# Optimization experiments

Hardware: AMD Instinct MI355X
Metric: run time of the kernel (lower is better)

The kernel has to match this reference:

```python
import jax, jax.numpy as jnp
import numpy as np

SIZE = 7
SIGMA = 1.5
K1 = 0.01
K2 = 0.03
DATA_RANGE = 2.0
NP_ = SIZE * SIZE
COV_NORM = NP_ / (NP_ - 1)
PAD = SIZE // 2


def _gaussian_window(size=SIZE, sigma=SIGMA, channels=1):
    x = np.arange(size) - size // 2
    g = np.exp(-x**2 / (2.0 * sigma**2))[None, :]
    g = (g.T @ g)
    g = g / g.sum()
    w = np.tile(g[None, None], (channels, 1, 1, 1))  # [C,1,size,size]
    return jnp.asarray(w, dtype=jnp.float32)


def _dwconv(x, w):
    # depthwise conv2d, zero padding PAD, stride 1; x: [N,C,H,W], w: [C,1,k,k]
    c = x.shape[1]
    return jax.lax.conv_general_dilated(
        x, w, window_strides=(1, 1), padding=[(PAD, PAD), (PAD, PAD)],
        dimension_numbers=('NCHW', 'OIHW', 'NCHW'), feature_group_count=c)


def setup_inputs() -> dict:
    key = jax.random.key(0)
    k1, k2 = jax.random.split(key)
    X = jax.random.uniform(k1, (64, 1, 320, 320), dtype=jnp.float32)
    Y = jax.random.uniform(k2, (64, 1, 320, 320), dtype=jnp.float32)
    window = _gaussian_window()
    return {"X": X, "Y": Y, "window": window}


def reference(X, Y, window):
    C1 = (K1 * DATA_RANGE) ** 2
    C2 = (K2 * DATA_RANGE) ** 2
    mux = _dwconv(X, window)
    muy = _dwconv(Y, window)
    mux_sq = mux * mux
    muy_sq = muy * muy
    muxy = mux * muy
    sigmax_sq = (_dwconv(X * X, window) - mux_sq) * COV_NORM
    sigmay_sq = (_dwconv(Y * Y, window) - muy_sq) * COV_NORM
    sigmaxy = (_dwconv(X * Y, window) - muxy) * COV_NORM
    ssim_map = ((2 * muxy + C1) * (2 * sigmaxy + C2)) / \
               ((mux_sq + muy_sq + C1) * (sigmax_sq + sigmay_sq + C2))
    return 1.0 - ssim_map.mean()
```

## Files before the change

kernel.cpp:

```cpp
#include <hip/hip_runtime.h>
#include <math.h>


#define WI 320
#define HI 320
#define NI 64
#define TWO 58
#define GXD 6
#define GYD 20
#define NBLK (GXD * GYD * NI)
#define NPIX ((double)NI * WI * HI)
#define WREG (5 * 4 * 64)

typedef float v4 __attribute__((ext_vector_type(4)));

struct W7 { float w[7]; };

template <bool YI, int XM>
__device__ __forceinline__ float wave_task(
    const float* __restrict__ Xn, const float* __restrict__ Yn,
    const W7& wv, float* __restrict__ vb, int x0, int y0, int lane)
{
    const int gx   = x0 + lane - 3;
    const bool xok = (XM == 1) || (XM == 0 ? (gx >= 0) : (gx < WI));

    float xr[10], yr[10];
#pragma unroll
    for (int j = 0; j < 10; ++j) {
        const int gy  = y0 + j - 3;
        const bool ok = xok && (YI || ((unsigned)gy < (unsigned)HI));
        float xv = 0.f, yv = 0.f;
        if (ok) { const int idx = gy * WI + gx; xv = Xn[idx]; yv = Yn[idx]; }
        xr[j] = xv; yr[j] = yv;
    }

    float acc[5][4];
#pragma unroll
    for (int ch = 0; ch < 5; ++ch)
#pragma unroll
        for (int r = 0; r < 4; ++r) acc[ch][r] = 0.f;
#pragma unroll
    for (int j = 0; j < 10; ++j) {
        const float xv = xr[j], yv = yr[j];
        const float pxx = xv * xv, pyy = yv * yv, pxy = xv * yv;
#pragma unroll
        for (int r = 0; r < 4; ++r) {
            const int d = j - r;
            if (d >= 0 && d < 7) {
                const float w = wv.w[d];
                acc[0][r] += w * xv;
                acc[1][r] += w * yv;
                acc[2][r] += w * pxx;
                acc[3][r] += w * pyy;
                acc[4][r] += w * pxy;
            }
        }
    }
#pragma unroll
    for (int ch = 0; ch < 5; ++ch)
#pragma unroll
        for (int r = 0; r < 4; ++r)
            vb[ch * 256 + r * 64 + lane] = acc[ch][r];

    __builtin_amdgcn_wave_barrier();

    float lsum = 0.f;
    const int row = lane >> 4;
    const int xg  = (lane & 15) << 2;
    if (xg < TWO) {
        const int xg3 = (xg > 52) ? 52 : xg;
        const float C1 = 0.0004f, C2 = 0.0036f, COVN = 49.f / 48.f;
        float m[4][5];
#pragma unroll
        for (int j = 0; j < 4; ++j)
#pragma unroll
            for (int ch = 0; ch < 5; ++ch) m[j][ch] = 0.f;
#pragma unroll
        for (int ch = 0; ch < 5; ++ch) {
            const float* base = &vb[ch * 256 + row * 64];
            v4 a = *(const v4*)&base[xg];
            v4 b = *(const v4*)&base[xg + 4];
            v4 c = *(const v4*)&base[xg3 + 8];
            float f[12] = {a.x,a.y,a.z,a.w, b.x,b.y,b.z,b.w, c.x,c.y,c.z,c.w};
#pragma unroll
            for (int j = 0; j < 4; ++j) {
                float s = 0.f;
#pragma unroll
                for (int d = 0; d < 7; ++d) s += wv.w[d] * f[j + d];
                m[j][ch] = s;
            }
        }
#pragma unroll
        for (int j = 0; j < 4; ++j) {
            const float mx = m[j][0], my = m[j][1];
            const float mxsq = mx * mx;
            const float mysq = my * my;
            const float mxy  = mx * my;
            const float vx   = (m[j][2] - mxsq) * COVN;
            const float vy   = (m[j][3] - mysq) * COVN;
            const float vxy  = (m[j][4] - mxy)  * COVN;
            const float num  = (2.f * mxy + C1) * (2.f * vxy + C2);
            const float den  = (mxsq + mysq + C1) * (vx + vy + C2);
            const bool valid = (xg + j < TWO) && (XM != 2 || x0 + xg + j < WI);
            lsum += valid ? num * __builtin_amdgcn_rcpf(den) : 0.f;
        }
    }
    return lsum;
}

__global__ __launch_bounds__(256, 7) void ssim_kernel(
    const float* __restrict__ X, const float* __restrict__ Y,
    W7 wv, float* __restrict__ partial)
{
    __shared__ __align__(16) float vbuf[4 * WREG];

    const int tid  = threadIdx.x;
    const int lane = tid & 63;
    const int w    = tid >> 6;
    const int x0   = blockIdx.x * TWO;
    const int y0   = blockIdx.y * 16 + w * 4;
    const float* __restrict__ Xn = X + (size_t)blockIdx.z * (WI * HI);
    const float* __restrict__ Yn = Y + (size_t)blockIdx.z * (WI * HI);
    float* vb = vbuf + w * WREG;

    const bool yi = (y0 >= 3) && (y0 <= HI - 7);
    const int  xm = (blockIdx.x == 0) ? 0 : ((blockIdx.x == GXD - 1) ? 2 : 1);

    float lsum;
    if (yi) {
        if      (xm == 0) lsum = wave_task<true, 0>(Xn, Yn, wv, vb, x0, y0, lane);
        else if (xm == 1) lsum = wave_task<true, 1>(Xn, Yn, wv, vb, x0, y0, lane);
        else              lsum = wave_task<true, 2>(Xn, Yn, wv, vb, x0, y0, lane);
    } else {
        if      (xm == 0) lsum = wave_task<false, 0>(Xn, Yn, wv, vb, x0, y0, lane);
        else if (xm == 1) lsum = wave_task<false, 1>(Xn, Yn, wv, vb, x0, y0, lane);
        else              lsum = wave_task<false, 2>(Xn, Yn, wv, vb, x0, y0, lane);
    }

#pragma unroll
    for (int off = 32; off > 0; off >>= 1)
        lsum += __shfl_down(lsum, off, 64);
    if (lane == 0) vbuf[w * WREG] = lsum;
    __syncthreads();
    if (tid == 0) {
        const int bid = (blockIdx.z * GYD + blockIdx.y) * GXD + blockIdx.x;
        partial[bid] = (vbuf[0] + vbuf[WREG]) + (vbuf[2 * WREG] + vbuf[3 * WREG]);
    }
}

__global__ __launch_bounds__(256) void ssim_finalize(
    const float* __restrict__ partial, float* __restrict__ out)
{
    __shared__ double ws[4];
    const int tid = threadIdx.x;
    double s = 0.0;
    for (int i = tid; i < NBLK; i += 256) s += (double)partial[i];
#pragma unroll
    for (int off = 32; off > 0; off >>= 1)
        s += __shfl_down(s, off, 64);
    if ((tid & 63) == 0) ws[tid >> 6] = s;
    __syncthreads();
    if (tid == 0)
        out[0] = (float)(1.0 - ((ws[0] + ws[1]) + (ws[2] + ws[3])) / NPIX);
}

extern "C" void kernel_launch(void* const* d_in, const int* in_sizes, int n_in,
                              void* d_out, int out_size, void* d_ws, size_t ws_size,
                              hipStream_t stream) {
    const float* X = (const float*)d_in[0];
    const float* Y = (const float*)d_in[1];
    W7 wv;
    {
        double g[7], s = 0.0;
        for (int i = 0; i < 7; ++i) {
            double x = (double)(i - 3);
            g[i] = exp(-(x * x) / (2.0 * 1.5 * 1.5));
            s += g[i];
        }
        for (int i = 0; i < 7; ++i) wv.w[i] = (float)(g[i] / s);
    }

    float* partial = (float*)d_ws;

    dim3 grid(GXD, GYD, NI);
    ssim_kernel<<<grid, 256, 0, stream>>>(X, Y, wv, partial);
    ssim_finalize<<<1, 256, 0, stream>>>(partial, (float*)d_out);
}
```

Measured before the change: 110.9 us.

## Process two images per block with packed float2 FMAs

Each block now handles a pair of images, and all arithmetic works on two-wide float vectors so the compiler can emit packed FP32 FMA instructions (v_pk_fma_f32) on CDNA. The grid z dimension is halved, shared memory per block doubles, and the occupancy hint drops from 7 to 4 blocks per CU. The aim is to cut VALU instruction count per pixel, at the cost of more registers, more LDS, and fewer resident waves to hide load latency.

```diff
diff --git a/kernel.cpp b/kernel.cpp
--- a/kernel.cpp
+++ b/kernel.cpp
@@ -5,54 +5,63 @@
 #define WI 320
 #define HI 320
 #define NI 64
+#define NZ (NI / 2)
 #define TWO 58
 #define GXD 6
 #define GYD 20
-#define NBLK (GXD * GYD * NI)
+#define NBLK (GXD * GYD * NZ)
+#define NPART (2 * NBLK)
 #define NPIX ((double)NI * WI * HI)
+#define IMG (WI * HI)
 #define WREG (5 * 4 * 64)
 
-typedef float v4 __attribute__((ext_vector_type(4)));
+typedef float v2f __attribute__((ext_vector_type(2)));
+typedef float v4f __attribute__((ext_vector_type(4)));
 
 struct W7 { float w[7]; };
 
 template <bool YI, int XM>
-__device__ __forceinline__ float wave_task(
-    const float* __restrict__ Xn, const float* __restrict__ Yn,
-    const W7& wv, float* __restrict__ vb, int x0, int y0, int lane)
+__device__ __forceinline__ v2f wave_task(
+    const float* __restrict__ X0, const float* __restrict__ X1,
+    const float* __restrict__ Y0, const float* __restrict__ Y1,
+    const W7& wv, v2f* __restrict__ vb, int x0, int y0, int lane)
 {
     const int gx   = x0 + lane - 3;
     const bool xok = (XM == 1) || (XM == 0 ? (gx >= 0) : (gx < WI));
 
-    float xr[10], yr[10];
+    v2f xr[10], yr[10];
 #pragma unroll
     for (int j = 0; j < 10; ++j) {
         const int gy  = y0 + j - 3;
         const bool ok = xok && (YI || ((unsigned)gy < (unsigned)HI));
-        float xv = 0.f, yv = 0.f;
-        if (ok) { const int idx = gy * WI + gx; xv = Xn[idx]; yv = Yn[idx]; }
+        v2f xv = {0.f, 0.f}, yv = {0.f, 0.f};
+        if (ok) {
+            const int idx = gy * WI + gx;
+            xv.x = X0[idx]; xv.y = X1[idx];
+            yv.x = Y0[idx]; yv.y = Y1[idx];
+        }
         xr[j] = xv; yr[j] = yv;
     }
 
-    float acc[5][4];
+    v2f acc[5][4];
 #pragma unroll
     for (int ch = 0; ch < 5; ++ch)
 #pragma unroll
-        for (int r = 0; r < 4; ++r) acc[ch][r] = 0.f;
+        for (int r = 0; r < 4; ++r) acc[ch][r] = (v2f){0.f, 0.f};
 #pragma unroll
     for (int j = 0; j < 10; ++j) {
-        const float xv = xr[j], yv = yr[j];
-        const float pxx = xv * xv, pyy = yv * yv, pxy = xv * yv;
+        const v2f xv = xr[j], yv = yr[j];
+        const v2f pxx = xv * xv, pyy = yv * yv, pxy = xv * yv;
 #pragma unroll
         for (int r = 0; r < 4; ++r) {
             const int d = j - r;
             if (d >= 0 && d < 7) {
-                const float w = wv.w[d];
-                acc[0][r] += w * xv;
-                acc[1][r] += w * yv;
-                acc[2][r] += w * pxx;
-                acc[3][r] += w * pyy;
-                acc[4][r] += w * pxy;
+                const v2f w2 = {wv.w[d], wv.w[d]};
+                acc[0][r] = __builtin_elementwise_fma(w2, xv,  acc[0][r]);
+                acc[1][r] = __builtin_elementwise_fma(w2, yv,  acc[1][r]);
+                acc[2][r] = __builtin_elementwise_fma(w2, pxx, acc[2][r]);
+                acc[3][r] = __builtin_elementwise_fma(w2, pyy, acc[3][r]);
+                acc[4][r] = __builtin_elementwise_fma(w2, pxy, acc[4][r]);
             }
         }
     }
@@ -64,87 +73,102 @@
 
     __builtin_amdgcn_wave_barrier();
 
-    float lsum = 0.f;
+    v2f lsum = {0.f, 0.f};
     const int row = lane >> 4;
     const int xg  = (lane & 15) << 2;
     if (xg < TWO) {
         const int xg3 = (xg > 52) ? 52 : xg;
-        const float C1 = 0.0004f, C2 = 0.0036f, COVN = 49.f / 48.f;
-        float m[4][5];
-#pragma unroll
-        for (int j = 0; j < 4; ++j)
-#pragma unroll
-            for (int ch = 0; ch < 5; ++ch) m[j][ch] = 0.f;
+        const v2f zero = {0.f, 0.f};
+        v2f m[4][5];
 #pragma unroll
         for (int ch = 0; ch < 5; ++ch) {
-            const float* base = &vb[ch * 256 + row * 64];
-            v4 a = *(const v4*)&base[xg];
-            v4 b = *(const v4*)&base[xg + 4];
-            v4 c = *(const v4*)&base[xg3 + 8];
-            float f[12] = {a.x,a.y,a.z,a.w, b.x,b.y,b.z,b.w, c.x,c.y,c.z,c.w};
+            const v2f* base = &vb[ch * 256 + row * 64];
+            const v4f q0 = *(const v4f*)&base[xg];
+            const v4f q1 = *(const v4f*)&base[xg + 2];
+            const v4f q2 = *(const v4f*)&base[xg + 4];
+            const v4f q3 = *(const v4f*)&base[xg + 6];
+            const v4f q4 = *(const v4f*)&base[xg3 + 8];
+            const v4f q5 = *(const v4f*)&base[xg3 + 10];
+            const v2f f2[12] = {
+                {q0.x,q0.y},{q0.z,q0.w},{q1.x,q1.y},{q1.z,q1.w},
+                {q2.x,q2.y},{q2.z,q2.w},{q3.x,q3.y},{q3.z,q3.w},
+                {q4.x,q4.y},{q4.z,q4.w},{q5.x,q5.y},{q5.z,q5.w}};
 #pragma unroll
             for (int j = 0; j < 4; ++j) {
-                float s = 0.f;
-#pragma unroll
-                for (int d = 0; d < 7; ++d) s += wv.w[d] * f[j + d];
+                v2f s = zero;
+#pragma unroll
+                for (int d = 0; d < 7; ++d) {
+                    const v2f w2 = {wv.w[d], wv.w[d]};
+                    s = __builtin_elementwise_fma(w2, f2[j + d], s);
+                }
                 m[j][ch] = s;
             }
         }
 #pragma unroll
         for (int j = 0; j < 4; ++j) {
-            const float mx = m[j][0], my = m[j][1];
-            const float mxsq = mx * mx;
-            const float mysq = my * my;
-            const float mxy  = mx * my;
-            const float vx   = (m[j][2] - mxsq) * COVN;
-            const float vy   = (m[j][3] - mysq) * COVN;
-            const float vxy  = (m[j][4] - mxy)  * COVN;
-            const float num  = (2.f * mxy + C1) * (2.f * vxy + C2);
-            const float den  = (mxsq + mysq + C1) * (vx + vy + C2);
+            const v2f mx = m[j][0], my = m[j][1];
+            const v2f mxsq = mx * mx;
+            const v2f mysq = my * my;
+            const v2f mxy  = mx * my;
+            const v2f vx   = (m[j][2] - mxsq) * 1.0208333333333333f;
+            const v2f vy   = (m[j][3] - mysq) * 1.0208333333333333f;
+            const v2f vxy  = (m[j][4] - mxy)  * 1.0208333333333333f;
+            const v2f num  = (2.f * mxy + 0.0004f) * (2.f * vxy + 0.0036f);
+            const v2f den  = (mxsq + mysq + 0.0004f) * (vx + vy + 0.0036f);
+            v2f rden;
+            rden.x = __builtin_amdgcn_rcpf(den.x);
+            rden.y = __builtin_amdgcn_rcpf(den.y);
+            const v2f term = num * rden;
             const bool valid = (xg + j < TWO) && (XM != 2 || x0 + xg + j < WI);
-            lsum += valid ? num * __builtin_amdgcn_rcpf(den) : 0.f;
+            lsum += valid ? term : zero;
         }
     }
     return lsum;
 }
 
-__global__ __launch_bounds__(256, 7) void ssim_kernel(
+__global__ __launch_bounds__(256, 4) void ssim_kernel(
     const float* __restrict__ X, const float* __restrict__ Y,
     W7 wv, float* __restrict__ partial)
 {
-    __shared__ __align__(16) float vbuf[4 * WREG];
+    __shared__ __align__(16) v2f vbuf[4 * WREG];
 
     const int tid  = threadIdx.x;
     const int lane = tid & 63;
     const int w    = tid >> 6;
     const int x0   = blockIdx.x * TWO;
     const int y0   = blockIdx.y * 16 + w * 4;
-    const float* __restrict__ Xn = X + (size_t)blockIdx.z * (WI * HI);
-    const float* __restrict__ Yn = Y + (size_t)blockIdx.z * (WI * HI);
-    float* vb = vbuf + w * WREG;
+    const float* __restrict__ X0 = X + (size_t)(2 * blockIdx.z) * IMG;
+    const float* __restrict__ X1 = X0 + IMG;
+    const float* __restrict__ Y0 = Y + (size_t)(2 * blockIdx.z) * IMG;
+    const float* __restrict__ Y1 = Y0 + IMG;
+    v2f* vb = vbuf + w * WREG;
 
     const bool yi = (y0 >= 3) && (y0 <= HI - 7);
     const int  xm = (blockIdx.x == 0) ? 0 : ((blockIdx.x == GXD - 1) ? 2 : 1);
 
-    float lsum;
+    v2f lsum;
     if (yi) {
-        if      (xm == 0) lsum = wave_task<true, 0>(Xn, Yn, wv, vb, x0, y0, lane);
-        else if (xm == 1) lsum = wave_task<true, 1>(Xn, Yn, wv, vb, x0, y0, lane);
-        else              lsum = wave_task<true, 2>(Xn, Yn, wv, vb, x0, y0, lane);
+        if      (xm == 0) lsum = wave_task<true, 0>(X0, X1, Y0, Y1, wv, vb, x0, y0, lane);
+        else if (xm == 1) lsum = wave_task<true, 1>(X0, X1, Y0, Y1, wv, vb, x0, y0, lane);
+        else              lsum = wave_task<true, 2>(X0, X1, Y0, Y1, wv, vb, x0, y0, lane);
     } else {
-        if      (xm == 0) lsum = wave_task<false, 0>(Xn, Yn, wv, vb, x0, y0, lane);
-        else if (xm == 1) lsum = wave_task<false, 1>(Xn, Yn, wv, vb, x0, y0, lane);
-        else              lsum = wave_task<false, 2>(Xn, Yn, wv, vb, x0, y0, lane);
-    }
-
-#pragma unroll
-    for (int off = 32; off > 0; off >>= 1)
-        lsum += __shfl_down(lsum, off, 64);
-    if (lane == 0) vbuf[w * WREG] = lsum;
+        if      (xm == 0) lsum = wave_task<false, 0>(X0, X1, Y0, Y1, wv, vb, x0, y0, lane);
+        else if (xm == 1) lsum = wave_task<false, 1>(X0, X1, Y0, Y1, wv, vb, x0, y0, lane);
+        else              lsum = wave_task<false, 2>(X0, X1, Y0, Y1, wv, vb, x0, y0, lane);
+    }
+
+#pragma unroll
+    for (int off = 32; off > 0; off >>= 1) {
+        lsum.x += __shfl_down(lsum.x, off, 64);
+        lsum.y += __shfl_down(lsum.y, off, 64);
+    }
+    if (lane == 0) vb[0] = lsum;
     __syncthreads();
     if (tid == 0) {
         const int bid = (blockIdx.z * GYD + blockIdx.y) * GXD + blockIdx.x;
-        partial[bid] = (vbuf[0] + vbuf[WREG]) + (vbuf[2 * WREG] + vbuf[3 * WREG]);
+        const v2f t = (vbuf[0] + vbuf[WREG]) + (vbuf[2 * WREG] + vbuf[3 * WREG]);
+        partial[2 * bid]     = t.x;
+        partial[2 * bid + 1] = t.y;
     }
 }
 
@@ -154,7 +178,7 @@
     __shared__ double ws[4];
     const int tid = threadIdx.x;
     double s = 0.0;
-    for (int i = tid; i < NBLK; i += 256) s += (double)partial[i];
+    for (int i = tid; i < NPART; i += 256) s += (double)partial[i];
 #pragma unroll
     for (int off = 32; off > 0; off >>= 1)
         s += __shfl_down(s, off, 64);
@@ -182,7 +206,7 @@
 
     float* partial = (float*)d_ws;
 
-    dim3 grid(GXD, GYD, NI);
+    dim3 grid(GXD, GYD, NZ);
     ssim_kernel<<<grid, 256, 0, stream>>>(X, Y, wv, partial);
     ssim_finalize<<<1, 256, 0, stream>>>(partial, (float*)d_out);
 }
```

New measurement: 106.7 us. -3.8%, faster.
